# Performance work log

Measured on AMD Instinct MI355X. Metric: run time of the kernel, lower is better.

The kernel has to match this reference:

```python
import jax, jax.numpy as jnp
import numpy as np

C = 128          # hidden_channels
H = 8            # num_heads
D = C // H       # head dim = 16
OUT = 64         # out_channels
L = 2            # num_layers
NN = (30000, 60000, 6000)                 # poi, road, region node counts
NE = (200000, 300000, 200000, 100000)     # edges per edge type
ETS = ((0, 1), (1, 1), (1, 2), (2, 0))    # (src_type, dst_type) per edge type


def setup_inputs():
    key = jax.random.key(0)
    ks = iter(jax.random.split(key, 40))
    s = 1.0 / np.sqrt(C)
    sd = 1.0 / np.sqrt(D)
    inp = {}
    inp['x_poi'] = jax.random.normal(next(ks), (NN[0], C), jnp.float32)
    inp['x_road'] = jax.random.normal(next(ks), (NN[1], C), jnp.float32)
    inp['x_region'] = jax.random.normal(next(ks), (NN[2], C), jnp.float32)
    for et, (si, di) in enumerate(ETS):
        inp[f'e{et}_src'] = jax.random.randint(next(ks), (NE[et],), 0, NN[si], jnp.int32)
        inp[f'e{et}_dst'] = jax.random.randint(next(ks), (NE[et],), 0, NN[di], jnp.int32)
    # per-node-type input projection
    inp['lin_w'] = jax.random.normal(next(ks), (3, C, C), jnp.float32) * s
    inp['lin_b'] = jax.random.normal(next(ks), (3, C), jnp.float32) * 0.01
    # per-layer, per-node-type K/Q/V and output projections
    for nm in ('kw', 'qw', 'vw', 'aw'):
        inp[nm] = jax.random.normal(next(ks), (L, 3, C, C), jnp.float32) * s
    for nm in ('kb', 'qb', 'vb', 'ab'):
        inp[nm] = jax.random.normal(next(ks), (L, 3, C), jnp.float32) * 0.01
    # per-layer, per-edge-type relation matrices and priors
    inp['a_rel'] = jax.random.normal(next(ks), (L, 4, H, D, D), jnp.float32) * sd
    inp['m_rel'] = jax.random.normal(next(ks), (L, 4, H, D, D), jnp.float32) * sd
    inp['p_rel'] = jnp.ones((L, 4, H), jnp.float32)
    inp['skip'] = jnp.ones((L, 3), jnp.float32)
    inp['out_w'] = jax.random.normal(next(ks), (C, OUT), jnp.float32) * s
    inp['out_b'] = jnp.zeros((OUT,), jnp.float32)
    return inp


def _seg_softmax(alpha, dst, n):
    amax = jax.lax.stop_gradient(jax.ops.segment_max(alpha, dst, num_segments=n))
    ex = jnp.exp(alpha - amax[dst])
    den = jax.ops.segment_sum(ex, dst, num_segments=n)
    return ex / (den[dst] + 1e-16)


def _hgt_forward(xs, edges, lin_w, lin_b, kw, kb, qw, qb, vw, vb, aw, ab,
                 a_rel, m_rel, p_rel, skip, out_w, out_b):
    # per-node-type input linear + relu
    xs = [jax.nn.relu(xs[i] @ lin_w[i] + lin_b[i]) for i in range(3)]
    scale = 1.0 / np.sqrt(D)
    for l in range(L):
        k = [(xs[i] @ kw[l, i] + kb[l, i]).reshape(-1, H, D) for i in range(3)]
        q = [(xs[i] @ qw[l, i] + qb[l, i]).reshape(-1, H, D) for i in range(3)]
        v = [(xs[i] @ vw[l, i] + vb[l, i]).reshape(-1, H, D) for i in range(3)]
        agg = [jnp.zeros((NN[i], H, D), xs[i].dtype) for i in range(3)]
        for et, (si, di) in enumerate(ETS):
            src, dst = edges[et]
            n = NN[di]
            ke = jnp.einsum('ehd,hdf->ehf', k[si][src], a_rel[l, et])   # [E,H,D]
            alpha = jnp.einsum('ehd,ehd->eh', q[di][dst], ke) * p_rel[l, et] * scale
            alpha = _seg_softmax(alpha, dst, n)                          # [E,H]
            m = jnp.einsum('ehd,hdf->ehf', v[si][src], m_rel[l, et])    # [E,H,D]
            agg[di] = agg[di] + jax.ops.segment_sum(m * alpha[..., None], dst, num_segments=n)
        new_xs = []
        for i in range(3):
            o = jax.nn.gelu(agg[i].reshape(-1, C)) @ aw[l, i] + ab[l, i]
            beta = jax.nn.sigmoid(skip[l, i])
            o = beta * o + (1.0 - beta) * xs[i]
            new_xs.append(jax.nn.relu(o))  # HGT applies activation after each conv
        xs = new_xs
    return (xs[0] @ out_w + out_b, xs[1] @ out_w + out_b, xs[2] @ out_w + out_b)


def reference(x_poi, x_road, x_region,
              e0_src, e0_dst, e1_src, e1_dst, e2_src, e2_dst, e3_src, e3_dst,
              lin_w, lin_b, kw, kb, qw, qb, vw, vb, aw, ab,
              a_rel, m_rel, p_rel, skip, out_w, out_b):
    edges = ((e0_src, e0_dst), (e1_src, e1_dst), (e2_src, e2_dst), (e3_src, e3_dst))
    return _hgt_forward([x_poi, x_road, x_region], edges,
                        lin_w, lin_b, kw, kb, qw, qb, vw, vb, aw, ab,
                        a_rel, m_rel, p_rel, skip, out_w, out_b)
```

## Files before the change

### kernel.cpp

```cpp
#include <hip/hip_runtime.h>
#include <cstddef>
#include <cstdint>


typedef __attribute__((ext_vector_type(8))) short short8;
typedef __attribute__((ext_vector_type(4))) float floatx4;

__device__ __forceinline__ float gelu_fast(float x) {
    float u = 1.5957691216057308f * x * (1.0f + 0.044715f * x * x);
    return x / (1.0f + __expf(-u));
}

__device__ __forceinline__ unsigned short f2bf(float f) {
    unsigned u = __float_as_uint(f);
    u += 0x7fffu + ((u >> 16) & 1);
    return (unsigned short)(u >> 16);
}

__device__ __forceinline__ float bf2f(unsigned short h) {
    return __uint_as_float((unsigned)h << 16);
}

__device__ __forceinline__ void up8(uint4 u, float* f) {
    f[0] = __uint_as_float(u.x << 16); f[1] = __uint_as_float(u.x & 0xffff0000u);
    f[2] = __uint_as_float(u.y << 16); f[3] = __uint_as_float(u.y & 0xffff0000u);
    f[4] = __uint_as_float(u.z << 16); f[5] = __uint_as_float(u.z & 0xffff0000u);
    f[6] = __uint_as_float(u.w << 16); f[7] = __uint_as_float(u.w & 0xffff0000u);
}

__device__ __forceinline__ uint4 pk8(const float* f) {
    uint4 u;
    u.x = (unsigned)f2bf(f[0]) | ((unsigned)f2bf(f[1]) << 16);
    u.y = (unsigned)f2bf(f[2]) | ((unsigned)f2bf(f[3]) << 16);
    u.z = (unsigned)f2bf(f[4]) | ((unsigned)f2bf(f[5]) << 16);
    u.w = (unsigned)f2bf(f[6]) | ((unsigned)f2bf(f[7]) << 16);
    return u;
}

__global__ __launch_bounds__(256, 2) void gemm_proj_all(
    const unsigned short* __restrict__ xs_bf,
    const unsigned short* __restrict__ Wl,
    const float* __restrict__ bl,
    unsigned short* __restrict__ proj)
{
    const int    NN_[3]  = {30000, 60000, 6000};
    const int    NPAN[3] = {469, 938, 94};
    const int    OFFr[3] = {0, 30000, 90000};
    const int    WOFF[3] = {0, 49152, 131072};
    const int    BOFF[3] = {0, 384, 1024};
    const size_t POFF[3] = {0, 11520000u, 49920000u};
    const int    LDO[3]  = {384, 640, 384};

    int b = blockIdx.x, t, cp, rb;
    if (b < 590)      { t = 1; cp = b / 118; rb = b - cp * 118; }
    else if (b < 767) { int lb = b - 590; t = 0; cp = lb / 59; rb = lb - cp * 59; }
    else              { int lb = b - 767; t = 2; cp = lb / 12; rb = lb - cp * 12; }
    int p0 = rb * 8, p1 = p0 + 8;
    if (p1 > NPAN[t]) p1 = NPAN[t];

    const unsigned short* Abf = xs_bf + (size_t)OFFr[t] * 128;
    const unsigned short* Wt  = Wl + WOFF[t];
    const float* bias = bl + BOFF[t] + cp * 128;
    unsigned short* outbf = proj + POFF[t];
    const int ldo = LDO[t], Nrows = NN_[t];

    const int wave = threadIdx.x >> 6, lane = threadIdx.x & 63;
    const int quad = lane >> 4, l16 = lane & 15;

    short8 B[2][4][4];
    {
        const unsigned short* wb = Wt + (size_t)(cp * 128 + l16) * 128 + quad * 8;
        #pragma unroll
        for (int T = 0; T < 2; ++T)
            #pragma unroll
            for (int c = 0; c < 4; ++c)
                #pragma unroll
                for (int kc = 0; kc < 4; ++kc)
                    B[T][c][kc] = *(const short8*)(wb + (size_t)(T * 64 + c * 16) * 128 + kc * 32);
    }
    float4 bv[2][4];
    #pragma unroll
    for (int T = 0; T < 2; ++T)
        #pragma unroll
        for (int c = 0; c < 4; ++c)
            bv[T][c] = *(const float4*)(bias + T * 64 + c * 16 + quad * 4);

    short8 Acur[4];
    {
        int m = p0 * 64 + wave * 16 + l16; if (m >= Nrows) m = Nrows - 1;
        const unsigned short* ap = Abf + (size_t)m * 128 + quad * 8;
        #pragma unroll
        for (int kc = 0; kc < 4; ++kc) Acur[kc] = *(const short8*)(ap + kc * 32);
    }
    for (int p = p0; p < p1; ++p) {
        short8 Anx[4];
        {
            int m = (p + 1) * 64 + wave * 16 + l16; if (m >= Nrows) m = Nrows - 1;
            const unsigned short* ap = Abf + (size_t)m * 128 + quad * 8;
            #pragma unroll
            for (int kc = 0; kc < 4; ++kc) Anx[kc] = *(const short8*)(ap + kc * 32);
        }
        floatx4 acc[2][4];
        #pragma unroll
        for (int T = 0; T < 2; ++T)
            #pragma unroll
            for (int c = 0; c < 4; ++c) acc[T][c] = (floatx4){0.f, 0.f, 0.f, 0.f};
        #pragma unroll
        for (int kc = 0; kc < 4; ++kc)
            #pragma unroll
            for (int T = 0; T < 2; ++T)
                #pragma unroll
                for (int c = 0; c < 4; ++c)
                    acc[T][c] = __builtin_amdgcn_mfma_f32_16x16x32_bf16(B[T][c][kc], Acur[kc], acc[T][c], 0, 0, 0);
        int node = p * 64 + wave * 16 + l16;
        if (node < Nrows) {
            unsigned short* op = outbf + (size_t)node * ldo + cp * 128 + quad * 4;
            #pragma unroll
            for (int T = 0; T < 2; ++T)
                #pragma unroll
                for (int c = 0; c < 4; ++c) {
                    uint2 u;
                    u.x = (unsigned)f2bf(acc[T][c][0] + bv[T][c].x) |
                          ((unsigned)f2bf(acc[T][c][1] + bv[T][c].y) << 16);
                    u.y = (unsigned)f2bf(acc[T][c][2] + bv[T][c].z) |
                          ((unsigned)f2bf(acc[T][c][3] + bv[T][c].w) << 16);
                    *(uint2*)(op + T * 64 + c * 16) = u;
                }
        }
        #pragma unroll
        for (int kc = 0; kc < 4; ++kc) Acur[kc] = Anx[kc];
    }
}

template<bool AF32, bool GIN, bool SKIP>
__global__ __launch_bounds__(256, 2) void gemm_node(
    const void* __restrict__ a0v, const void* __restrict__ a1v, const void* __restrict__ a2v,
    const unsigned short* __restrict__ WtB, const float* __restrict__ biasB,
    const unsigned short* __restrict__ xoldB, const float* __restrict__ skipB,
    unsigned short* __restrict__ outB)
{
    const int TN[3]   = {30000, 60000, 6000};
    const int NPAN[3] = {469, 938, 94};
    const int TOFF[3] = {0, 30000, 90000};
    int b = blockIdx.x, t, rb;
    if (b < 235)      { t = 0; rb = b; }
    else if (b < 704) { t = 1; rb = b - 235; }
    else              { t = 2; rb = b - 704; }
    int p0 = rb * 2, p1 = p0 + 2;
    if (p1 > NPAN[t]) p1 = NPAN[t];
    int Nrows = TN[t];
    const void* av = (t == 0) ? a0v : (t == 1) ? a1v : a2v;
    const unsigned short* xold = xoldB + (size_t)TOFF[t] * 128;
    unsigned short* out = outB + (size_t)TOFF[t] * 128;

    const int wave = threadIdx.x >> 6, lane = threadIdx.x & 63;
    const int quad = lane >> 4, l16 = lane & 15;

    short8 B[8][4];
    {
        const unsigned short* wb = WtB + (size_t)t * 16384 + (size_t)l16 * 128 + quad * 8;
        #pragma unroll
        for (int c = 0; c < 8; ++c)
            #pragma unroll
            for (int kc = 0; kc < 4; ++kc)
                B[c][kc] = *(const short8*)(wb + (size_t)c * 2048 + kc * 32);
    }
    float beta = 0.f, omb = 0.f;
    if (SKIP) { beta = 1.0f / (1.0f + __expf(-skipB[t])); omb = 1.0f - beta; }

    short8 Acur[4];
    {
        int m = p0 * 64 + wave * 16 + l16; if (m >= Nrows) m = Nrows - 1;
        size_t base = (size_t)m * 128 + quad * 8;
        #pragma unroll
        for (int kc = 0; kc < 4; ++kc) {
            if (AF32) {
                const float* ap = (const float*)av + base;
                float4 f0 = *(const float4*)(ap + kc * 32);
                float4 f1 = *(const float4*)(ap + kc * 32 + 4);
                float af[8] = {f0.x, f0.y, f0.z, f0.w, f1.x, f1.y, f1.z, f1.w};
                short8 a;
                #pragma unroll
                for (int i = 0; i < 8; ++i) a[i] = (short)f2bf(af[i]);
                Acur[kc] = a;
            } else if (GIN) {
                const unsigned short* ap = (const unsigned short*)av + base;
                short8 a8 = *(const short8*)(ap + kc * 32);
                short8 a;
                #pragma unroll
                for (int i = 0; i < 8; ++i)
                    a[i] = (short)f2bf(gelu_fast(bf2f((unsigned short)a8[i])));
                Acur[kc] = a;
            } else {
                const unsigned short* ap = (const unsigned short*)av + base;
                Acur[kc] = *(const short8*)(ap + kc * 32);
            }
        }
    }
    for (int p = p0; p < p1; ++p) {
        float4 Fnx[4][2];
        short8 Snx[4];
        {
            int m = (p + 1) * 64 + wave * 16 + l16; if (m >= Nrows) m = Nrows - 1;
            size_t base = (size_t)m * 128 + quad * 8;
            #pragma unroll
            for (int kc = 0; kc < 4; ++kc) {
                if (AF32) {
                    const float* ap = (const float*)av + base;
                    Fnx[kc][0] = *(const float4*)(ap + kc * 32);
                    Fnx[kc][1] = *(const float4*)(ap + kc * 32 + 4);
                } else {
                    const unsigned short* ap = (const unsigned short*)av + base;
                    Snx[kc] = *(const short8*)(ap + kc * 32);
                }
            }
        }
        int node = p * 64 + wave * 16 + l16;
        int ncl = (node < Nrows) ? node : (Nrows - 1);
        uint2 xo[8];
        if (SKIP) {
            #pragma unroll
            for (int c = 0; c < 8; ++c)
                xo[c] = *(const uint2*)(xold + (size_t)ncl * 128 + c * 16 + quad * 4);
        }
        floatx4 acc[8];
        #pragma unroll
        for (int c = 0; c < 8; ++c) acc[c] = (floatx4){0.f, 0.f, 0.f, 0.f};
        #pragma unroll
        for (int kc = 0; kc < 4; ++kc)
            #pragma unroll
            for (int c = 0; c < 8; ++c)
                acc[c] = __builtin_amdgcn_mfma_f32_16x16x32_bf16(B[c][kc], Acur[kc], acc[c], 0, 0, 0);
        if (node < Nrows) {
            #pragma unroll
            for (int c = 0; c < 8; ++c) {
                int col0 = c * 16 + quad * 4;
                float4 bv = *(const float4*)(biasB + t * 128 + col0);
                float o0 = acc[c][0] + bv.x, o1 = acc[c][1] + bv.y;
                float o2 = acc[c][2] + bv.z, o3 = acc[c][3] + bv.w;
                if (SKIP) {
                    o0 = beta * o0 + omb * __uint_as_float(xo[c].x << 16);
                    o1 = beta * o1 + omb * __uint_as_float(xo[c].x & 0xffff0000u);
                    o2 = beta * o2 + omb * __uint_as_float(xo[c].y << 16);
                    o3 = beta * o3 + omb * __uint_as_float(xo[c].y & 0xffff0000u);
                }
                o0 = fmaxf(o0, 0.f); o1 = fmaxf(o1, 0.f);
                o2 = fmaxf(o2, 0.f); o3 = fmaxf(o3, 0.f);
                uint2 u;
                u.x = (unsigned)f2bf(o0) | ((unsigned)f2bf(o1) << 16);
                u.y = (unsigned)f2bf(o2) | ((unsigned)f2bf(o3) << 16);
                *(uint2*)(out + (size_t)node * 128 + col0) = u;
            }
        }
        #pragma unroll
        for (int kc = 0; kc < 4; ++kc) {
            if (AF32) {
                float af[8] = {Fnx[kc][0].x, Fnx[kc][0].y, Fnx[kc][0].z, Fnx[kc][0].w,
                               Fnx[kc][1].x, Fnx[kc][1].y, Fnx[kc][1].z, Fnx[kc][1].w};
                short8 a;
                #pragma unroll
                for (int i = 0; i < 8; ++i) a[i] = (short)f2bf(af[i]);
                Acur[kc] = a;
            } else if (GIN) {
                short8 a;
                #pragma unroll
                for (int i = 0; i < 8; ++i)
                    a[i] = (short)f2bf(gelu_fast(bf2f((unsigned short)Snx[kc][i])));
                Acur[kc] = a;
            } else {
                Acur[kc] = Snx[kc];
            }
        }
    }
}

__global__ __launch_bounds__(256, 3) void gemm_out(
    const unsigned short* __restrict__ Abf,
    const unsigned short* __restrict__ Wt,
    const float* __restrict__ bias,
    float* __restrict__ out, int Nrows)
{
    const int wave = threadIdx.x >> 6, lane = threadIdx.x & 63;
    const int quad = lane >> 4, l16 = lane & 15;
    int p0 = blockIdx.x * 4, p1 = p0 + 4;

    short8 B[4][4];
    {
        const unsigned short* wb = Wt + (size_t)l16 * 128 + quad * 8;
        #pragma unroll
        for (int c = 0; c < 4; ++c)
            #pragma unroll
            for (int kc = 0; kc < 4; ++kc)
                B[c][kc] = *(const short8*)(wb + (size_t)c * 2048 + kc * 32);
    }
    float4 bv[4];
    #pragma unroll
    for (int c = 0; c < 4; ++c) bv[c] = *(const float4*)(bias + c * 16 + quad * 4);

    short8 Acur[4];
    {
        int m = p0 * 64 + wave * 16 + l16; if (m >= Nrows) m = Nrows - 1;
        const unsigned short* ap = Abf + (size_t)m * 128 + quad * 8;
        #pragma unroll
        for (int kc = 0; kc < 4; ++kc) Acur[kc] = *(const short8*)(ap + kc * 32);
    }
    for (int p = p0; p < p1; ++p) {
        short8 Anx[4];
        {
            int m = (p + 1) * 64 + wave * 16 + l16; if (m >= Nrows) m = Nrows - 1;
            const unsigned short* ap = Abf + (size_t)m * 128 + quad * 8;
            #pragma unroll
            for (int kc = 0; kc < 4; ++kc) Anx[kc] = *(const short8*)(ap + kc * 32);
        }
        floatx4 acc[4];
        #pragma unroll
        for (int c = 0; c < 4; ++c) acc[c] = (floatx4){0.f, 0.f, 0.f, 0.f};
        #pragma unroll
        for (int kc = 0; kc < 4; ++kc)
            #pragma unroll
            for (int c = 0; c < 4; ++c)
                acc[c] = __builtin_amdgcn_mfma_f32_16x16x32_bf16(B[c][kc], Acur[kc], acc[c], 0, 0, 0);
        int node = p * 64 + wave * 16 + l16;
        if (node < Nrows) {
            #pragma unroll
            for (int c = 0; c < 4; ++c) {
                float4 o;
                o.x = acc[c][0] + bv[c].x; o.y = acc[c][1] + bv[c].y;
                o.z = acc[c][2] + bv[c].z; o.w = acc[c][3] + bv[c].w;
                *(float4*)(out + (size_t)node * 64 + c * 16 + quad * 4) = o;
            }
        }
        #pragma unroll
        for (int kc = 0; kc < 4; ++kc) Acur[kc] = Anx[kc];
    }
}

__global__ __launch_bounds__(128) void prep_all(
    const float* __restrict__ qw, const float* __restrict__ qb,
    const float* __restrict__ kw, const float* __restrict__ kb,
    const float* __restrict__ vw, const float* __restrict__ vb,
    const float* __restrict__ a_rel, const float* __restrict__ m_rel,
    const float* __restrict__ lin_w, const float* __restrict__ aw,
    const float* __restrict__ ow,
    unsigned short* __restrict__ Wpack, float* __restrict__ bpack,
    unsigned short* __restrict__ lwt, unsigned short* __restrict__ awt,
    unsigned short* __restrict__ owt)
{
    const int pre[3] = {0, 49152, 131072};
    const int preB[3] = {0, 384, 1024};
    int b = blockIdx.x;
    if (b < 768) {
        int n = threadIdx.x;
        int k = b & 127, r = b >> 7, t = r % 3, l = r / 3;
        unsigned short* Wp = Wpack + (size_t)l * 180224 + pre[t];
        Wp[(size_t)n * 128 + k] = f2bf(qw[(size_t)(l * 3 + t) * 16384 + (size_t)k * 128 + n]);
        if (k == 0) bpack[l * 1408 + preB[t] + n] = qb[(l * 3 + t) * 128 + n];
    } else if (b < 1792) {
        const int SIv[4] = {0, 1, 1, 2};
        const int SLOT[4] = {0, 0, 1, 0};
        int bb = b - 768;
        int hf = threadIdx.x, h = hf >> 4, f = hf & 15;
        int c = bb & 127, et = (bb >> 7) & 3, l = bb >> 9;
        int si = SIv[et];
        const float* kwp  = kw + (size_t)(l * 3 + si) * 16384;
        const float* vwp  = vw + (size_t)(l * 3 + si) * 16384;
        const float* kbp  = kb + (size_t)(l * 3 + si) * 128;
        const float* vbp  = vb + (size_t)(l * 3 + si) * 128;
        const float* arel = a_rel + (size_t)(l * 4 + et) * 2048;
        const float* mrel = m_rel + (size_t)(l * 4 + et) * 2048;
        float sk = 0.f, sv = 0.f;
        #pragma unroll
        for (int d = 0; d < 16; ++d) {
            float ar = arel[(h * 16 + d) * 16 + f];
            float mr = mrel[(h * 16 + d) * 16 + f];
            sk = fmaf(kwp[c * 128 + h * 16 + d], ar, sk);
            sv = fmaf(vwp[c * 128 + h * 16 + d], mr, sv);
        }
        int rowoff = 128 + 256 * SLOT[et];
        unsigned short* Wp = Wpack + (size_t)l * 180224 + pre[si];
        Wp[(size_t)(rowoff + hf) * 128 + c]       = f2bf(sk);
        Wp[(size_t)(rowoff + 128 + hf) * 128 + c] = f2bf(sv);
        if (c == 0) {
            float bk = 0.f, bvv = 0.f;
            #pragma unroll
            for (int d = 0; d < 16; ++d) {
                bk  = fmaf(kbp[h * 16 + d], arel[(h * 16 + d) * 16 + f], bk);
                bvv = fmaf(vbp[h * 16 + d], mrel[(h * 16 + d) * 16 + f], bvv);
            }
            float* bp = bpack + l * 1408 + preB[si];
            bp[rowoff + hf]       = bk;
            bp[rowoff + 128 + hf] = bvv;
        }
    } else if (b < 2944) {
        int bb = b - 1792;
        int n = threadIdx.x, k = bb & 127, mi = bb >> 7;
        const float* w; unsigned short* wt; int m;
        if (mi < 3) { w = lin_w; wt = lwt; m = mi; }
        else        { w = aw;    wt = awt; m = mi - 3; }
        wt[(size_t)m * 16384 + (size_t)n * 128 + k] =
            f2bf(w[(size_t)m * 16384 + (size_t)k * 128 + n]);
    } else {
        int k = b - 2944, n = threadIdx.x;
        if (n < 64) owt[(size_t)n * 128 + k] = f2bf(ow[(size_t)k * 64 + n]);
    }
}

__global__ __launch_bounds__(256) void hist_all(
    const int* __restrict__ d0, const int* __restrict__ d1,
    const int* __restrict__ d2, const int* __restrict__ d3,
    int* __restrict__ deg4)
{
    const int Ev[4] = {200000, 300000, 200000, 100000};
    int et = blockIdx.y;
    int e = blockIdx.x * 256 + threadIdx.x;
    if (e >= Ev[et]) return;
    const int* d = et == 0 ? d0 : et == 1 ? d1 : et == 2 ? d2 : d3;
    atomicAdd(&deg4[et * 60000 + d[e]], 1);
}

__global__ __launch_bounds__(256) void scan_tile_all(
    const int* __restrict__ deg4,
    int* __restrict__ r0, int* __restrict__ r1, int* __restrict__ r2, int* __restrict__ r3,
    int* __restrict__ tsum4)
{
    const int Ndv[4] = {60000, 60000, 6000, 30000};
    __shared__ int ls[256];
    int et = blockIdx.y;
    int n = Ndv[et];
    const int* deg = deg4 + et * 60000;
    int* rowptr = et == 0 ? r0 : et == 1 ? r1 : et == 2 ? r2 : r3;
    int b = blockIdx.x, tid = threadIdx.x;
    int base = b * 1024 + tid * 4;
    int v0 = 0, v1 = 0, v2 = 0, v3 = 0;
    if (base + 3 < n) {
        int4 t = *(const int4*)(deg + base);
        v0 = t.x; v1 = t.y; v2 = t.z; v3 = t.w;
    } else {
        if (base + 0 < n) v0 = deg[base + 0];
        if (base + 1 < n) v1 = deg[base + 1];
        if (base + 2 < n) v2 = deg[base + 2];
        if (base + 3 < n) v3 = deg[base + 3];
    }
    int s = v0 + v1 + v2 + v3;
    ls[tid] = s;
    __syncthreads();
    #pragma unroll
    for (int off = 1; off < 256; off <<= 1) {
        int t = (tid >= off) ? ls[tid - off] : 0;
        __syncthreads();
        ls[tid] += t;
        __syncthreads();
    }
    int run = ls[tid] - s;
    int o0 = run; run += v0;
    int o1 = run; run += v1;
    int o2 = run; run += v2;
    int o3 = run;
    if (base + 3 < n) {
        *(int4*)(rowptr + base) = make_int4(o0, o1, o2, o3);
    } else {
        if (base + 0 < n) rowptr[base + 0] = o0;
        if (base + 1 < n) rowptr[base + 1] = o1;
        if (base + 2 < n) rowptr[base + 2] = o2;
    }
    if (tid == 255) tsum4[et * 64 + b] = ls[255];
}

__global__ __launch_bounds__(64) void scan_tsum_all(
    int* __restrict__ tsum4,
    int* __restrict__ r0, int* __restrict__ r1, int* __restrict__ r2, int* __restrict__ r3)
{
    const int Ndv[4] = {60000, 60000, 6000, 30000};
    int et = blockIdx.x;
    int n = Ndv[et];
    int nt = (n + 1023) >> 10;
    int* tileSum = tsum4 + et * 64;
    int* rowptr = et == 0 ? r0 : et == 1 ? r1 : et == 2 ? r2 : r3;
    int tid = threadIdx.x;
    int v = (tid < nt) ? tileSum[tid] : 0;
    int orig = v;
    #pragma unroll
    for (int off = 1; off < 64; off <<= 1) {
        int t = __shfl_up(v, off);
        if (tid >= off) v += t;
    }
    if (tid < nt) tileSum[tid] = v - orig;
    if (tid == nt - 1) rowptr[n] = v;
}

__global__ __launch_bounds__(256) void scan_add_all(
    int* __restrict__ r0, int* __restrict__ r1, int* __restrict__ r2, int* __restrict__ r3,
    const int* __restrict__ tsum4)
{
    const int Ndv[4] = {60000, 60000, 6000, 30000};
    int et = blockIdx.y;
    int n = Ndv[et];
    int* rowptr = et == 0 ? r0 : et == 1 ? r1 : et == 2 ? r2 : r3;
    int i = blockIdx.x * 256 + threadIdx.x;
    if (i < n) rowptr[i] += tsum4[et * 64 + (i >> 10)];
}

__global__ __launch_bounds__(256) void fill_all(
    const int* __restrict__ s0, const int* __restrict__ d0,
    const int* __restrict__ s1, const int* __restrict__ d1,
    const int* __restrict__ s2, const int* __restrict__ d2,
    const int* __restrict__ s3, const int* __restrict__ d3,
    const int* __restrict__ r0, const int* __restrict__ r1,
    const int* __restrict__ r2, const int* __restrict__ r3,
    int* __restrict__ deg4,
    int* __restrict__ c0, int* __restrict__ c1, int* __restrict__ c2, int* __restrict__ c3)
{
    const int Ev[4] = {200000, 300000, 200000, 100000};
    int et = blockIdx.y;
    int e = blockIdx.x * 256 + threadIdx.x;
    if (e >= Ev[et]) return;
    const int* src = et == 0 ? s0 : et == 1 ? s1 : et == 2 ? s2 : s3;
    const int* dst = et == 0 ? d0 : et == 1 ? d1 : et == 2 ? d2 : d3;
    const int* rowptr = et == 0 ? r0 : et == 1 ? r1 : et == 2 ? r2 : r3;
    int* csr = et == 0 ? c0 : et == 1 ? c1 : et == 2 ? c2 : c3;
    int d = dst[e];
    int pos = atomicAdd(&deg4[et * 60000 + d], 1);
    csr[rowptr[d] + pos] = src[e];
}

__device__ __forceinline__ int perm_key(
    const int* rp0, const int* rp1, const int* rp2, const int* rp3,
    int sec, int i)
{
    int d;
    if (sec == 0)      d = (rp0[i + 1] - rp0[i]) + (rp1[i + 1] - rp1[i]);
    else if (sec == 1) d = rp3[i + 1] - rp3[i];
    else               d = rp2[i + 1] - rp2[i];
    return d < 511 ? d : 511;
}

__global__ __launch_bounds__(256) void perm_hist(
    const int* __restrict__ rp0, const int* __restrict__ rp1,
    const int* __restrict__ rp2, const int* __restrict__ rp3,
    int* __restrict__ hist)
{
    const int N[3] = {60000, 30000, 6000};
    __shared__ int lh[512];
    int sec = blockIdx.y, tid = threadIdx.x;
    lh[tid] = 0; lh[tid + 256] = 0;
    __syncthreads();
    int i = blockIdx.x * 256 + tid;
    if (i < N[sec])
        atomicAdd(&lh[perm_key(rp0, rp1, rp2, rp3, sec, i)], 1);
    __syncthreads();
    if (lh[tid])       atomicAdd(&hist[sec * 512 + tid],       lh[tid]);
    if (lh[tid + 256]) atomicAdd(&hist[sec * 512 + tid + 256], lh[tid + 256]);
}

__global__ __launch_bounds__(512) void perm_scan(int* __restrict__ hist)
{
    __shared__ int ls[512];
    int* h = hist + blockIdx.x * 512;
    int tid = threadIdx.x;
    int v = h[tid];
    ls[tid] = v;
    __syncthreads();
    for (int off = 1; off < 512; off <<= 1) {
        int t = (tid >= off) ? ls[tid - off] : 0;
        __syncthreads();
        ls[tid] += t;
        __syncthreads();
    }
    h[tid] = ls[tid] - v;
}

__global__ __launch_bounds__(256) void perm_scatter(
    const int* __restrict__ rp0, const int* __restrict__ rp1,
    const int* __restrict__ rp2, const int* __restrict__ rp3,
    int* __restrict__ hist,
    int* __restrict__ permR, int* __restrict__ permP, int* __restrict__ permG)
{
    const int N[3] = {60000, 30000, 6000};
    __shared__ int lh[512];
    __shared__ int lofs[512];
    int sec = blockIdx.y, tid = threadIdx.x;
    lh[tid] = 0; lh[tid + 256] = 0;
    __syncthreads();
    int i = blockIdx.x * 256 + tid;
    int d = -1, lrank = 0;
    if (i < N[sec]) {
        d = perm_key(rp0, rp1, rp2, rp3, sec, i);
        lrank = atomicAdd(&lh[d], 1);
    }
    __syncthreads();
    if (lh[tid])       lofs[tid]       = atomicAdd(&hist[sec * 512 + tid],       lh[tid]);
    if (lh[tid + 256]) lofs[tid + 256] = atomicAdd(&hist[sec * 512 + tid + 256], lh[tid + 256]);
    __syncthreads();
    if (i < N[sec]) {
        int* perm = (sec == 0) ? permR : (sec == 1) ? permP : permG;
        perm[lofs[d] + lrank] = i;
    }
}

__device__ __forceinline__ void attn_edge(
    uint4 k0, uint4 k1, uint4 v0, uint4 v1,
    const float* qf, float ph, float& m, float& l, float* o)
{
    float kf[16];
    up8(k0, kf); up8(k1, kf + 8);
    float a = 0.f;
    #pragma unroll
    for (int i = 0; i < 16; ++i) a = fmaf(qf[i], kf[i], a);
    a *= ph;
    float d = a - m;
    if (d > 8.f) {
        float sc = __expf(-d);
        l *= sc;
        #pragma unroll
        for (int i = 0; i < 16; ++i) o[i] *= sc;
        m = a; d = 0.f;
    }
    float w = __expf(d);
    l += w;
    float vf[16];
    up8(v0, vf); up8(v1, vf + 8);
    #pragma unroll
    for (int i = 0; i < 16; ++i) o[i] = fmaf(w, vf[i], o[i]);
}

__device__ __forceinline__ void attn_run(
    const int* __restrict__ csr, int beg, int end,
    const unsigned short* __restrict__ kbase, int ld,
    const float* qf, float ph, float& m, float& l, float* o)
{
    int n = end - beg;
    if (n <= 0) return;
    const uint4* pA = (const uint4*)(kbase + (size_t)csr[beg] * ld);
    uint4 A0 = pA[0], A1 = pA[1], A2 = pA[16], A3 = pA[17];
    uint4 B0 = A0, B1 = A1, B2 = A2, B3 = A3;
    if (n > 1) {
        const uint4* pB = (const uint4*)(kbase + (size_t)csr[beg + 1] * ld);
        B0 = pB[0]; B1 = pB[1]; B2 = pB[16]; B3 = pB[17];
    }
    int j = beg;
    for (; j + 3 < end; j += 2) {
        const uint4* pC = (const uint4*)(kbase + (size_t)csr[j + 2] * ld);
        const uint4* pD = (const uint4*)(kbase + (size_t)csr[j + 3] * ld);
        uint4 C0 = pC[0], C1 = pC[1], C2 = pC[16], C3 = pC[17];
        uint4 D0 = pD[0], D1 = pD[1], D2 = pD[16], D3 = pD[17];
        float kf0[16], kf1[16];
        up8(A0, kf0); up8(A1, kf0 + 8);
        up8(B0, kf1); up8(B1, kf1 + 8);
        float a0 = 0.f, a1 = 0.f;
        #pragma unroll
        for (int i = 0; i < 16; ++i) {
            a0 = fmaf(qf[i], kf0[i], a0);
            a1 = fmaf(qf[i], kf1[i], a1);
        }
        a0 *= ph; a1 *= ph;
        float hi = fmaxf(a0, a1);
        float d = hi - m;
        if (d > 8.f) {
            float sc = __expf(-d);
            l *= sc;
            #pragma unroll
            for (int i = 0; i < 16; ++i) o[i] *= sc;
            m = hi;
        }
        float w0 = __expf(a0 - m), w1 = __expf(a1 - m);
        l += w0 + w1;
        float vf0[16], vf1[16];
        up8(A2, vf0); up8(A3, vf0 + 8);
        up8(B2, vf1); up8(B3, vf1 + 8);
        #pragma unroll
        for (int i = 0; i < 16; ++i)
            o[i] = fmaf(w1, vf1[i], fmaf(w0, vf0[i], o[i]));
        A0 = C0; A1 = C1; A2 = C2; A3 = C3;
        B0 = D0; B1 = D1; B2 = D2; B3 = D3;
    }
    int rem = end - j;
    attn_edge(A0, A1, A2, A3, qf, ph, m, l, o);
    if (rem >= 2) attn_edge(B0, B1, B2, B3, qf, ph, m, l, o);
    if (rem == 3) {
        const uint4* pC = (const uint4*)(kbase + (size_t)csr[j + 2] * ld);
        attn_edge(pC[0], pC[1], pC[16], pC[17], qf, ph, m, l, o);
    }
}

__device__ __forceinline__ void merge_sm(float& m, float& l, float* o, int st)
{
    float mp = __shfl_xor(m, st);
    float lp = __shfl_xor(l, st);
    float mn = fmaxf(m, mp);
    float sc  = (l  > 0.f) ? __expf(m  - mn) : 0.f;
    float scp = (lp > 0.f) ? __expf(mp - mn) : 0.f;
    l = l * sc + lp * scp;
    #pragma unroll
    for (int i = 0; i < 16; ++i) {
        float op = __shfl_xor(o[i], st);
        o[i] = o[i] * sc + op * scp;
    }
    m = mn;
}

__global__ __launch_bounds__(256) void agg_all(
    const int* __restrict__ rp0, const int* __restrict__ cs0,
    const int* __restrict__ rp1, const int* __restrict__ cs1,
    const int* __restrict__ rp2, const int* __restrict__ cs2,
    const int* __restrict__ rp3, const int* __restrict__ cs3,
    const unsigned short* __restrict__ P0, const unsigned short* __restrict__ P1,
    const unsigned short* __restrict__ P2,
    const float* __restrict__ prl,
    const int* __restrict__ pmR, const int* __restrict__ pmP,
    const int* __restrict__ pmG,
    unsigned short* __restrict__ num)
{
    int gb = blockIdx.x, tid = threadIdx.x;
    float qf[16], o[16], r[16];
    if (gb < 3750) {
        int t = gb * 256 + tid;
        int node = pmR[59999 - (t >> 4)], h = t & 7, half = (t >> 3) & 1;
        const uint4* qp = (const uint4*)(P1 + (size_t)node * 640 + h * 16);
        up8(qp[0], qf); up8(qp[1], qf + 8);
        int beg = rp0[node], end = rp0[node + 1], n = end - beg;
        int b0 = beg + ((n * half) >> 1), e0 = beg + ((n * (half + 1)) >> 1);
        float m0 = -INFINITY, l0 = 0.f;
        #pragma unroll
        for (int i = 0; i < 16; ++i) o[i] = 0.f;
        attn_run(cs0, b0, e0, P0 + 128 + h * 16, 384,
                 qf, prl[h] * 0.25f, m0, l0, o);
        merge_sm(m0, l0, o, 8);
        float i0 = 1.f / (l0 + 1e-16f);
        #pragma unroll
        for (int i = 0; i < 16; ++i) { r[i] = i0 * o[i]; o[i] = 0.f; }
        beg = rp1[node]; end = rp1[node + 1]; n = end - beg;
        b0 = beg + ((n * half) >> 1); e0 = beg + ((n * (half + 1)) >> 1);
        float m1 = -INFINITY, l1 = 0.f;
        attn_run(cs1, b0, e0, P1 + 128 + h * 16, 640,
                 qf, prl[8 + h] * 0.25f, m1, l1, o);
        merge_sm(m1, l1, o, 8);
        float i1 = 1.f / (l1 + 1e-16f);
        #pragma unroll
        for (int i = 0; i < 16; ++i) r[i] += i1 * o[i];
        if (half) return;
        uint4* np = (uint4*)(num + (size_t)(30000 + node) * 128 + h * 16);
        np[0] = pk8(r); np[1] = pk8(r + 8);
    } else if (gb < 4500) {
        int t = (gb - 3750) * 256 + tid;
        int node = pmG[5999 - (t >> 5)], h = t & 7, sub = (t >> 3) & 3;
        int beg0 = rp2[node], end0 = rp2[node + 1];
        int n = end0 - beg0;
        int beg = beg0 + ((n * sub) >> 2);
        int end = beg0 + ((n * (sub + 1)) >> 2);
        const uint4* qp = (const uint4*)(P2 + (size_t)node * 384 + h * 16);
        up8(qp[0], qf); up8(qp[1], qf + 8);
        float m = -INFINITY, l = 0.f;
        #pragma unroll
        for (int i = 0; i < 16; ++i) o[i] = 0.f;
        attn_run(cs2, beg, end, P1 + 384 + h * 16, 640,
                 qf, prl[16 + h] * 0.25f, m, l, o);
        merge_sm(m, l, o, 8);
        merge_sm(m, l, o, 16);
        if (sub) return;
        float inv = 1.f / (l + 1e-16f);
        #pragma unroll
        for (int i = 0; i < 16; ++i) r[i] = inv * o[i];
        uint4* np = (uint4*)(num + (size_t)(90000 + node) * 128 + h * 16);
        np[0] = pk8(r); np[1] = pk8(r + 8);
    } else {
        int t = (gb - 4500) * 256 + tid;
        int node = pmP[29999 - (t >> 4)], h = t & 7, half = (t >> 3) & 1;
        int beg = rp3[node], end = rp3[node + 1], n = end - beg;
        int b0 = beg + ((n * half) >> 1), e0 = beg + ((n * (half + 1)) >> 1);
        const uint4* qp = (const uint4*)(P0 + (size_t)node * 384 + h * 16);
        up8(qp[0], qf); up8(qp[1], qf + 8);
        float m = -INFINITY, l = 0.f;
        #pragma unroll
        for (int i = 0; i < 16; ++i) o[i] = 0.f;
        attn_run(cs3, b0, e0, P2 + 128 + h * 16, 384,
                 qf, prl[24 + h] * 0.25f, m, l, o);
        merge_sm(m, l, o, 8);
        if (half) return;
        float inv = 1.f / (l + 1e-16f);
        #pragma unroll
        for (int i = 0; i < 16; ++i) r[i] = inv * o[i];
        uint4* np = (uint4*)(num + (size_t)node * 128 + h * 16);
        np[0] = pk8(r); np[1] = pk8(r + 8);
    }
}

extern "C" void kernel_launch(void* const* d_in, const int* in_sizes, int n_in,
                              void* d_out, int out_size, void* d_ws, size_t ws_size,
                              hipStream_t stream)
{
    (void)in_sizes; (void)n_in; (void)out_size; (void)ws_size;

    const float* xin[3] = {(const float*)d_in[0], (const float*)d_in[1], (const float*)d_in[2]};
    const int* esrc[4] = {(const int*)d_in[3], (const int*)d_in[5], (const int*)d_in[7], (const int*)d_in[9]};
    const int* edst[4] = {(const int*)d_in[4], (const int*)d_in[6], (const int*)d_in[8], (const int*)d_in[10]};
    const float* lin_w = (const float*)d_in[11];
    const float* lin_b = (const float*)d_in[12];
    const float* kw = (const float*)d_in[13];
    const float* qw = (const float*)d_in[14];
    const float* vw = (const float*)d_in[15];
    const float* aw = (const float*)d_in[16];
    const float* kb = (const float*)d_in[17];
    const float* qb = (const float*)d_in[18];
    const float* vb = (const float*)d_in[19];
    const float* ab = (const float*)d_in[20];
    const float* a_rel = (const float*)d_in[21];
    const float* m_rel = (const float*)d_in[22];
    const float* p_rel = (const float*)d_in[23];
    const float* skip  = (const float*)d_in[24];
    const float* out_w = (const float*)d_in[25];
    const float* out_b = (const float*)d_in[26];

    float* ws = (float*)d_ws;
    unsigned short* num   = (unsigned short*)ws;
    unsigned short* xs_bf = (unsigned short*)(ws + 6144000);
    unsigned short* proj  = (unsigned short*)(ws + 12288000);
    unsigned short* Wpack = (unsigned short*)(ws + 38400000);
    unsigned short* lwt   = (unsigned short*)(ws + 38580224);
    unsigned short* awt   = (unsigned short*)(ws + 38604800);
    unsigned short* owt   = (unsigned short*)(ws + 38653952);
    float*          bpack = ws + 38658048;
    int*            deg4  = (int*)(ws + 38660864);
    int*            tsum4 = (int*)(ws + 38900864);
    int* rp[4];
    rp[0] = (int*)(ws + 38901120);
    rp[1] = (int*)(ws + 38961128);
    rp[2] = (int*)(ws + 39021136);
    rp[3] = (int*)(ws + 39027144);
    int* cs[4];
    cs[0] = (int*)(ws + 39057152);
    cs[1] = (int*)(ws + 39257152);
    cs[2] = (int*)(ws + 39557152);
    cs[3] = (int*)(ws + 39757152);
    int* permR = deg4;
    int* permP = deg4 + 60000;
    int* permG = deg4 + 90000;
    int* phist = deg4 + 96000;

    unsigned short* P[3];
    P[0] = proj;
    P[1] = proj + (size_t)30000 * 384;
    P[2] = proj + (size_t)30000 * 384 + (size_t)60000 * 640;

    dim3 blk(256);

    hipMemsetAsync(deg4, 0, 960000, stream);
    hist_all<<<dim3(1172, 4), blk, 0, stream>>>(edst[0], edst[1], edst[2], edst[3], deg4);
    scan_tile_all<<<dim3(59, 4), blk, 0, stream>>>(deg4, rp[0], rp[1], rp[2], rp[3], tsum4);
    scan_tsum_all<<<dim3(4), dim3(64), 0, stream>>>(tsum4, rp[0], rp[1], rp[2], rp[3]);
    scan_add_all<<<dim3(235, 4), blk, 0, stream>>>(rp[0], rp[1], rp[2], rp[3], tsum4);
    hipMemsetAsync(deg4, 0, 960000, stream);
    fill_all<<<dim3(1172, 4), blk, 0, stream>>>(
        esrc[0], edst[0], esrc[1], edst[1], esrc[2], edst[2], esrc[3], edst[3],
        rp[0], rp[1], rp[2], rp[3], deg4, cs[0], cs[1], cs[2], cs[3]);

    hipMemsetAsync(phist, 0, 1536 * 4, stream);
    perm_hist<<<dim3(235, 3), blk, 0, stream>>>(rp[0], rp[1], rp[2], rp[3], phist);
    perm_scan<<<dim3(3), dim3(512), 0, stream>>>(phist);
    perm_scatter<<<dim3(235, 3), blk, 0, stream>>>(
        rp[0], rp[1], rp[2], rp[3], phist, permR, permP, permG);

    prep_all<<<dim3(3072), dim3(128), 0, stream>>>(
        qw, qb, kw, kb, vw, vb, a_rel, m_rel, lin_w, aw, out_w,
        Wpack, bpack, lwt, awt, owt);

    gemm_node<true, false, false><<<dim3(751), blk, 0, stream>>>(
        xin[0], xin[1], xin[2], lwt, lin_b, nullptr, nullptr, xs_bf);

    for (int l = 0; l < 2; ++l) {
        gemm_proj_all<<<dim3(803), blk, 0, stream>>>(
            xs_bf, Wpack + (size_t)l * 180224, bpack + l * 1408, proj);

        agg_all<<<dim3(6375), blk, 0, stream>>>(
            rp[0], cs[0], rp[1], cs[1], rp[2], cs[2], rp[3], cs[3],
            P[0], P[1], P[2], p_rel + (size_t)l * 32,
            permR, permP, permG, num);

        gemm_node<false, true, true><<<dim3(751), blk, 0, stream>>>(
            num, num + (size_t)30000 * 128, num + (size_t)90000 * 128,
            awt + (size_t)l * 3 * 16384, ab + (size_t)l * 3 * 128,
            xs_bf, skip + l * 3, xs_bf);
    }

    gemm_out<<<dim3(375), blk, 0, stream>>>(
        xs_bf, owt, out_b, (float*)d_out, 96000);
}
```

Before: 599.8 us.

## Drop degree-sorted node permutation, fold scan stages, simplify agg work split

Removes the degree-bucketed permutation kernels (hist/scan/scatter) and the separate tile-sum scan kernel plus one memset. scan_tile_all now zeroes the degree counts as it reads them, and scan_add_all computes the tile prefix itself. In agg_all, road nodes give each edge type to one half-wave and combine the halves with a shuffle, and POI nodes now use one thread group per node instead of splitting edges in half. Fewer launches and less setup work, at the cost of losing degree-sorted load balancing in the aggregation.

```diff
diff --git a/kernel.cpp b/kernel.cpp
--- a/kernel.cpp
+++ b/kernel.cpp
@@ -419,7 +419,7 @@
 }
 
 __global__ __launch_bounds__(256) void scan_tile_all(
-    const int* __restrict__ deg4,
+    int* __restrict__ deg4,
     int* __restrict__ r0, int* __restrict__ r1, int* __restrict__ r2, int* __restrict__ r3,
     int* __restrict__ tsum4)
 {
@@ -427,7 +427,7 @@
     __shared__ int ls[256];
     int et = blockIdx.y;
     int n = Ndv[et];
-    const int* deg = deg4 + et * 60000;
+    int* deg = deg4 + et * 60000;
     int* rowptr = et == 0 ? r0 : et == 1 ? r1 : et == 2 ? r2 : r3;
     int b = blockIdx.x, tid = threadIdx.x;
     int base = b * 1024 + tid * 4;
@@ -435,11 +435,12 @@
     if (base + 3 < n) {
         int4 t = *(const int4*)(deg + base);
         v0 = t.x; v1 = t.y; v2 = t.z; v3 = t.w;
+        *(int4*)(deg + base) = make_int4(0, 0, 0, 0);
     } else {
-        if (base + 0 < n) v0 = deg[base + 0];
-        if (base + 1 < n) v1 = deg[base + 1];
-        if (base + 2 < n) v2 = deg[base + 2];
-        if (base + 3 < n) v3 = deg[base + 3];
+        if (base + 0 < n) { v0 = deg[base + 0]; deg[base + 0] = 0; }
+        if (base + 1 < n) { v1 = deg[base + 1]; deg[base + 1] = 0; }
+        if (base + 2 < n) { v2 = deg[base + 2]; deg[base + 2] = 0; }
+        if (base + 3 < n) { v3 = deg[base + 3]; deg[base + 3] = 0; }
     }
     int s = v0 + v1 + v2 + v3;
     ls[tid] = s;
@@ -466,38 +467,28 @@
     if (tid == 255) tsum4[et * 64 + b] = ls[255];
 }
 
-__global__ __launch_bounds__(64) void scan_tsum_all(
-    int* __restrict__ tsum4,
-    int* __restrict__ r0, int* __restrict__ r1, int* __restrict__ r2, int* __restrict__ r3)
-{
-    const int Ndv[4] = {60000, 60000, 6000, 30000};
-    int et = blockIdx.x;
-    int n = Ndv[et];
-    int nt = (n + 1023) >> 10;
-    int* tileSum = tsum4 + et * 64;
-    int* rowptr = et == 0 ? r0 : et == 1 ? r1 : et == 2 ? r2 : r3;
-    int tid = threadIdx.x;
-    int v = (tid < nt) ? tileSum[tid] : 0;
-    int orig = v;
-    #pragma unroll
-    for (int off = 1; off < 64; off <<= 1) {
-        int t = __shfl_up(v, off);
-        if (tid >= off) v += t;
-    }
-    if (tid < nt) tileSum[tid] = v - orig;
-    if (tid == nt - 1) rowptr[n] = v;
-}
-
 __global__ __launch_bounds__(256) void scan_add_all(
     int* __restrict__ r0, int* __restrict__ r1, int* __restrict__ r2, int* __restrict__ r3,
     const int* __restrict__ tsum4)
 {
     const int Ndv[4] = {60000, 60000, 6000, 30000};
+    __shared__ int ts[64];
     int et = blockIdx.y;
     int n = Ndv[et];
     int* rowptr = et == 0 ? r0 : et == 1 ? r1 : et == 2 ? r2 : r3;
-    int i = blockIdx.x * 256 + threadIdx.x;
-    if (i < n) rowptr[i] += tsum4[et * 64 + (i >> 10)];
+    int tid = threadIdx.x;
+    if (tid < 64) ts[tid] = tsum4[et * 64 + tid];
+    __syncthreads();
+    int i = blockIdx.x * 256 + tid;
+    int tile = i >> 10;
+    int pre = 0;
+    for (int j = 0; j < tile; ++j) pre += ts[j];
+    if (i < n) rowptr[i] += pre;
+    if (blockIdx.x == 0 && tid == 0) {
+        int nt = (n + 1023) >> 10, tot = 0;
+        for (int j = 0; j < nt; ++j) tot += ts[j];
+        rowptr[n] = tot;
+    }
 }
 
 __global__ __launch_bounds__(256) void fill_all(
@@ -523,80 +514,6 @@
     csr[rowptr[d] + pos] = src[e];
 }
 
-__device__ __forceinline__ int perm_key(
-    const int* rp0, const int* rp1, const int* rp2, const int* rp3,
-    int sec, int i)
-{
-    int d;
-    if (sec == 0)      d = (rp0[i + 1] - rp0[i]) + (rp1[i + 1] - rp1[i]);
-    else if (sec == 1) d = rp3[i + 1] - rp3[i];
-    else               d = rp2[i + 1] - rp2[i];
-    return d < 511 ? d : 511;
-}
-
-__global__ __launch_bounds__(256) void perm_hist(
-    const int* __restrict__ rp0, const int* __restrict__ rp1,
-    const int* __restrict__ rp2, const int* __restrict__ rp3,
-    int* __restrict__ hist)
-{
-    const int N[3] = {60000, 30000, 6000};
-    __shared__ int lh[512];
-    int sec = blockIdx.y, tid = threadIdx.x;
-    lh[tid] = 0; lh[tid + 256] = 0;
-    __syncthreads();
-    int i = blockIdx.x * 256 + tid;
-    if (i < N[sec])
-        atomicAdd(&lh[perm_key(rp0, rp1, rp2, rp3, sec, i)], 1);
-    __syncthreads();
-    if (lh[tid])       atomicAdd(&hist[sec * 512 + tid],       lh[tid]);
-    if (lh[tid + 256]) atomicAdd(&hist[sec * 512 + tid + 256], lh[tid + 256]);
-}
-
-__global__ __launch_bounds__(512) void perm_scan(int* __restrict__ hist)
-{
-    __shared__ int ls[512];
-    int* h = hist + blockIdx.x * 512;
-    int tid = threadIdx.x;
-    int v = h[tid];
-    ls[tid] = v;
-    __syncthreads();
-    for (int off = 1; off < 512; off <<= 1) {
-        int t = (tid >= off) ? ls[tid - off] : 0;
-        __syncthreads();
-        ls[tid] += t;
-        __syncthreads();
-    }
-    h[tid] = ls[tid] - v;
-}
-
-__global__ __launch_bounds__(256) void perm_scatter(
-    const int* __restrict__ rp0, const int* __restrict__ rp1,
-    const int* __restrict__ rp2, const int* __restrict__ rp3,
-    int* __restrict__ hist,
-    int* __restrict__ permR, int* __restrict__ permP, int* __restrict__ permG)
-{
-    const int N[3] = {60000, 30000, 6000};
-    __shared__ int lh[512];
-    __shared__ int lofs[512];
-    int sec = blockIdx.y, tid = threadIdx.x;
-    lh[tid] = 0; lh[tid + 256] = 0;
-    __syncthreads();
-    int i = blockIdx.x * 256 + tid;
-    int d = -1, lrank = 0;
-    if (i < N[sec]) {
-        d = perm_key(rp0, rp1, rp2, rp3, sec, i);
-        lrank = atomicAdd(&lh[d], 1);
-    }
-    __syncthreads();
-    if (lh[tid])       lofs[tid]       = atomicAdd(&hist[sec * 512 + tid],       lh[tid]);
-    if (lh[tid + 256]) lofs[tid + 256] = atomicAdd(&hist[sec * 512 + tid + 256], lh[tid + 256]);
-    __syncthreads();
-    if (i < N[sec]) {
-        int* perm = (sec == 0) ? permR : (sec == 1) ? permP : permG;
-        perm[lofs[d] + lrank] = i;
-    }
-}
-
 __device__ __forceinline__ void attn_edge(
     uint4 k0, uint4 k1, uint4 v0, uint4 v1,
     const float* qf, float ph, float& m, float& l, float* o)
@@ -706,43 +623,35 @@
     const unsigned short* __restrict__ P0, const unsigned short* __restrict__ P1,
     const unsigned short* __restrict__ P2,
     const float* __restrict__ prl,
-    const int* __restrict__ pmR, const int* __restrict__ pmP,
-    const int* __restrict__ pmG,
     unsigned short* __restrict__ num)
 {
     int gb = blockIdx.x, tid = threadIdx.x;
     float qf[16], o[16], r[16];
     if (gb < 3750) {
         int t = gb * 256 + tid;
-        int node = pmR[59999 - (t >> 4)], h = t & 7, half = (t >> 3) & 1;
+        int node = t >> 4, h = t & 7, half = (t >> 3) & 1;
         const uint4* qp = (const uint4*)(P1 + (size_t)node * 640 + h * 16);
         up8(qp[0], qf); up8(qp[1], qf + 8);
-        int beg = rp0[node], end = rp0[node + 1], n = end - beg;
-        int b0 = beg + ((n * half) >> 1), e0 = beg + ((n * (half + 1)) >> 1);
-        float m0 = -INFINITY, l0 = 0.f;
+        const int* csr = half ? cs1 : cs0;
+        const int* rp  = half ? rp1 : rp0;
+        const unsigned short* kb = half ? (P1 + 128 + h * 16) : (P0 + 128 + h * 16);
+        int ld = half ? 640 : 384;
+        float ph = prl[(half ? 8 : 0) + h] * 0.25f;
+        float m = -INFINITY, l = 0.f;
         #pragma unroll
         for (int i = 0; i < 16; ++i) o[i] = 0.f;
-        attn_run(cs0, b0, e0, P0 + 128 + h * 16, 384,
-                 qf, prl[h] * 0.25f, m0, l0, o);
-        merge_sm(m0, l0, o, 8);
-        float i0 = 1.f / (l0 + 1e-16f);
-        #pragma unroll
-        for (int i = 0; i < 16; ++i) { r[i] = i0 * o[i]; o[i] = 0.f; }
-        beg = rp1[node]; end = rp1[node + 1]; n = end - beg;
-        b0 = beg + ((n * half) >> 1); e0 = beg + ((n * (half + 1)) >> 1);
-        float m1 = -INFINITY, l1 = 0.f;
-        attn_run(cs1, b0, e0, P1 + 128 + h * 16, 640,
-                 qf, prl[8 + h] * 0.25f, m1, l1, o);
-        merge_sm(m1, l1, o, 8);
-        float i1 = 1.f / (l1 + 1e-16f);
-        #pragma unroll
-        for (int i = 0; i < 16; ++i) r[i] += i1 * o[i];
+        attn_run(csr, rp[node], rp[node + 1], kb, ld, qf, ph, m, l, o);
+        float inv = 1.f / (l + 1e-16f);
+        #pragma unroll
+        for (int i = 0; i < 16; ++i) r[i] = inv * o[i];
+        #pragma unroll
+        for (int i = 0; i < 16; ++i) r[i] += __shfl_xor(r[i], 8);
         if (half) return;
         uint4* np = (uint4*)(num + (size_t)(30000 + node) * 128 + h * 16);
         np[0] = pk8(r); np[1] = pk8(r + 8);
     } else if (gb < 4500) {
         int t = (gb - 3750) * 256 + tid;
-        int node = pmG[5999 - (t >> 5)], h = t & 7, sub = (t >> 3) & 3;
+        int node = t >> 5, h = t & 7, sub = (t >> 3) & 3;
         int beg0 = rp2[node], end0 = rp2[node + 1];
         int n = end0 - beg0;
         int beg = beg0 + ((n * sub) >> 2);
@@ -764,18 +673,15 @@
         np[0] = pk8(r); np[1] = pk8(r + 8);
     } else {
         int t = (gb - 4500) * 256 + tid;
-        int node = pmP[29999 - (t >> 4)], h = t & 7, half = (t >> 3) & 1;
-        int beg = rp3[node], end = rp3[node + 1], n = end - beg;
-        int b0 = beg + ((n * half) >> 1), e0 = beg + ((n * (half + 1)) >> 1);
+        if (t >= 240000) return;
+        int node = t >> 3, h = t & 7;
         const uint4* qp = (const uint4*)(P0 + (size_t)node * 384 + h * 16);
         up8(qp[0], qf); up8(qp[1], qf + 8);
         float m = -INFINITY, l = 0.f;
         #pragma unroll
         for (int i = 0; i < 16; ++i) o[i] = 0.f;
-        attn_run(cs3, b0, e0, P2 + 128 + h * 16, 384,
+        attn_run(cs3, rp3[node], rp3[node + 1], P2 + 128 + h * 16, 384,
                  qf, prl[24 + h] * 0.25f, m, l, o);
-        merge_sm(m, l, o, 8);
-        if (half) return;
         float inv = 1.f / (l + 1e-16f);
         #pragma unroll
         for (int i = 0; i < 16; ++i) r[i] = inv * o[i];
@@ -831,10 +737,6 @@
     cs[1] = (int*)(ws + 39257152);
     cs[2] = (int*)(ws + 39557152);
     cs[3] = (int*)(ws + 39757152);
-    int* permR = deg4;
-    int* permP = deg4 + 60000;
-    int* permG = deg4 + 90000;
-    int* phist = deg4 + 96000;
 
     unsigned short* P[3];
     P[0] = proj;
@@ -846,19 +748,11 @@
     hipMemsetAsync(deg4, 0, 960000, stream);
     hist_all<<<dim3(1172, 4), blk, 0, stream>>>(edst[0], edst[1], edst[2], edst[3], deg4);
     scan_tile_all<<<dim3(59, 4), blk, 0, stream>>>(deg4, rp[0], rp[1], rp[2], rp[3], tsum4);
-    scan_tsum_all<<<dim3(4), dim3(64), 0, stream>>>(tsum4, rp[0], rp[1], rp[2], rp[3]);
     scan_add_all<<<dim3(235, 4), blk, 0, stream>>>(rp[0], rp[1], rp[2], rp[3], tsum4);
-    hipMemsetAsync(deg4, 0, 960000, stream);
     fill_all<<<dim3(1172, 4), blk, 0, stream>>>(
         esrc[0], edst[0], esrc[1], edst[1], esrc[2], edst[2], esrc[3], edst[3],
         rp[0], rp[1], rp[2], rp[3], deg4, cs[0], cs[1], cs[2], cs[3]);
 
-    hipMemsetAsync(phist, 0, 1536 * 4, stream);
-    perm_hist<<<dim3(235, 3), blk, 0, stream>>>(rp[0], rp[1], rp[2], rp[3], phist);
-    perm_scan<<<dim3(3), dim3(512), 0, stream>>>(phist);
-    perm_scatter<<<dim3(235, 3), blk, 0, stream>>>(
-        rp[0], rp[1], rp[2], rp[3], phist, permR, permP, permG);
-
     prep_all<<<dim3(3072), dim3(128), 0, stream>>>(
         qw, qb, kw, kb, vw, vb, a_rel, m_rel, lin_w, aw, out_w,
         Wpack, bpack, lwt, awt, owt);
@@ -870,10 +764,9 @@
         gemm_proj_all<<<dim3(803), blk, 0, stream>>>(
             xs_bf, Wpack + (size_t)l * 180224, bpack + l * 1408, proj);
 
-        agg_all<<<dim3(6375), blk, 0, stream>>>(
+        agg_all<<<dim3(5438), blk, 0, stream>>>(
             rp[0], cs[0], rp[1], cs[1], rp[2], cs[2], rp[3], cs[3],
-            P[0], P[1], P[2], p_rel + (size_t)l * 32,
-            permR, permP, permG, num);
+            P[0], P[1], P[2], p_rel + (size_t)l * 32, num);
 
         gemm_node<false, true, true><<<dim3(751), blk, 0, stream>>>(
             num, num + (size_t)30000 * 128, num + (size_t)90000 * 128,
```

Result: faster. 567.1 us (-5.4%).
